# Kernel tuning notes

Hardware: AMD Instinct MI355X
Metric: run time of the kernel (lower is better)

The kernel has to match this reference:

```python
import jax, jax.numpy as jnp
import numpy as np

HEAD = 16
EMB = 1024
D_K = EMB // HEAD


def setup_inputs() -> dict:
    key = jax.random.key(0)
    ks = jax.random.split(key, 11)
    B, S, E = 2, 2048, EMB
    scale = 1.0 / np.sqrt(E)
    inp = {
        "query": jax.random.normal(ks[0], (B, S, E), jnp.float32),
        "key": jax.random.normal(ks[1], (B, S, E), jnp.float32),
        "value": jax.random.normal(ks[2], (B, S, E), jnp.float32),
        "Wq": jax.random.normal(ks[3], (E, E), jnp.float32) * scale,
        "bq": jnp.zeros((E,), jnp.float32),
        "Wk": jax.random.normal(ks[4], (E, E), jnp.float32) * scale,
        "bk": jnp.zeros((E,), jnp.float32),
        "Wv": jax.random.normal(ks[5], (E, E), jnp.float32) * scale,
        "bv": jnp.zeros((E,), jnp.float32),
        "Wo": jax.random.normal(ks[6], (E, E), jnp.float32) * scale,
        "bo": jnp.zeros((E,), jnp.float32),
    }
    return inp


def reference(query, key, value, Wq, bq, Wk, bk, Wv, bv, Wo, bo):
    B, S, E = query.shape
    # 3 input projections, split into heads: [B, H, S, d_k]
    def proj(x, W, b):
        return (x @ W.T + b).reshape(B, S, HEAD, D_K).transpose(0, 2, 1, 3)

    q = proj(query, Wq, bq)
    k = proj(key, Wk, bk)
    v = proj(value, Wv, bv)

    # scaled dot-product attention (full matrix, as in original)
    scores = jnp.einsum("bhqd,bhkd->bhqk", q, k) / jnp.sqrt(jnp.float32(D_K))
    attn = jax.nn.softmax(scores, axis=-1)  # dropout in eval mode = identity
    x = jnp.einsum("bhqk,bhkd->bhqd", attn, v)

    # merge heads and output projection
    x = x.transpose(0, 2, 1, 3).reshape(B, S, E)
    return x @ Wo.T + bo
```

## Files before the change

### kernel.cpp

```cpp
#include <hip/hip_runtime.h>
#include <hip/hip_bf16.h>
#include <math.h>


constexpr int Sn = 2048;
constexpr int En = 1024;
constexpr int Hn = 16;
constexpr int Dk = 64;
constexpr int Kn = 1024;
constexpr size_t WSZ = 1048576;
constexpr size_t TSZ = 4194304;
constexpr int PST = 72;

typedef __bf16 bf16x8 __attribute__((ext_vector_type(8)));
typedef float  f32x4  __attribute__((ext_vector_type(4)));

union U16 { uint4 u; bf16x8 v; __hip_bfloat16 h[8]; };
union U8  { uint2 u; __hip_bfloat162 h2[2]; __hip_bfloat16 h[4]; };

__device__ inline U16 cvt8f(const float* __restrict__ p) {
    float4 a = *(const float4*)p;
    float4 b = *(const float4*)(p + 4);
    U16 r;
    r.h[0] = __float2bfloat16(a.x); r.h[1] = __float2bfloat16(a.y);
    r.h[2] = __float2bfloat16(a.z); r.h[3] = __float2bfloat16(a.w);
    r.h[4] = __float2bfloat16(b.x); r.h[5] = __float2bfloat16(b.y);
    r.h[6] = __float2bfloat16(b.z); r.h[7] = __float2bfloat16(b.w);
    return r;
}

__device__ inline void gload16(const __hip_bfloat16* g, __hip_bfloat16* l) {
    __builtin_amdgcn_global_load_lds(
        (const __attribute__((address_space(1))) void*)g,
        (__attribute__((address_space(3))) void*)l, 16, 0, 0);
}

template<int ROWS, int NW>
__device__ inline void stage_tile(const __hip_bfloat16* __restrict__ src, int ld,
                                  __hip_bfloat16* lds, int w, int lane) {
    int l8 = lane >> 3;
    int g = (lane & 7) ^ (l8 & 7);
    #pragma unroll
    for (int j = 0; j < ROWS / (8 * NW); ++j) {
        int c = j * NW + w;
        gload16(src + (size_t)(c * 8 + l8) * ld + g * 8, lds + c * 512);
    }
}

__global__ __launch_bounds__(256)
void cvt_w(const float* __restrict__ w0, const float* __restrict__ w1,
           const float* __restrict__ w2, const float* __restrict__ w3,
           __hip_bfloat16* __restrict__ dst)
{
    int y = blockIdx.y;
    const float* src = (y == 0) ? w0 : (y == 1) ? w1 : (y == 2) ? w2 : w3;
    size_t i = ((size_t)blockIdx.x * 256 + threadIdx.x) * 8;
    U16 r = cvt8f(src + i);
    *(uint4*)&dst[(size_t)y * WSZ + i] = r.u;
}

__global__ __launch_bounds__(256)
void qkv_gemm(const float* __restrict__ xq, const float* __restrict__ xk,
              const float* __restrict__ xv, const __hip_bfloat16* __restrict__ Wbf,
              const float* __restrict__ bq, const float* __restrict__ bk,
              const float* __restrict__ bv,
              __hip_bfloat16* __restrict__ Qw, __hip_bfloat16* __restrict__ Kw,
              __hip_bfloat16* __restrict__ Vtw)
{
    __shared__ __align__(16) __hip_bfloat16 As[128 * 64];
    __shared__ __align__(16) __hip_bfloat16 Bs[128 * 64];

    const int tid = threadIdx.x, w = tid >> 6, lane = tid & 63;
    const int l15 = lane & 15, lg = lane >> 4, l7 = lane & 7;
    const int z = blockIdx.z;
    const float* A    = (z == 0) ? xq : (z == 1) ? xk : xv;
    const float* bias = (z == 0) ? bq : (z == 1) ? bk : bv;
    const __hip_bfloat16* W = Wbf + (size_t)z * WSZ;
    const int blockM = blockIdx.x * 128, blockN = blockIdx.y * 128;
    const int wm = (w & 1) * 64, wn = (w >> 1) * 64;

    const int arow = tid >> 1, acb = (tid & 1) * 4;
    const int coff0 = (lg ^ l7) * 8;
    const int coff1 = ((4 + lg) ^ l7) * 8;

    f32x4 acc[4][4];
    #pragma unroll
    for (int i = 0; i < 4; ++i)
        #pragma unroll
        for (int j = 0; j < 4; ++j) acc[i][j] = {0.f, 0.f, 0.f, 0.f};

    for (int k0 = 0; k0 < Kn; k0 += 64) {
        {
            const float* ap = A + (size_t)(blockM + arow) * Kn + k0 + acb * 8;
            int s7 = arow & 7;
            #pragma unroll
            for (int g = 0; g < 4; ++g) {
                U16 r = cvt8f(ap + g * 8);
                *(uint4*)&As[arow * 64 + (((acb + g) ^ s7) * 8)] = r.u;
            }
        }
        stage_tile<128, 4>(W + (size_t)blockN * Kn + k0, Kn, Bs, w, lane);
        __syncthreads();

        U16 af[4][2], bf[4][2];
        #pragma unroll
        for (int mt = 0; mt < 4; ++mt) {
            int r = (wm + mt * 16 + l15) * 64;
            af[mt][0].u = *(const uint4*)&As[r + coff0];
            af[mt][1].u = *(const uint4*)&As[r + coff1];
        }
        #pragma unroll
        for (int nt = 0; nt < 4; ++nt) {
            int r = (wn + nt * 16 + l15) * 64;
            bf[nt][0].u = *(const uint4*)&Bs[r + coff0];
            bf[nt][1].u = *(const uint4*)&Bs[r + coff1];
        }
        #pragma unroll
        for (int mt = 0; mt < 4; ++mt)
            #pragma unroll
            for (int nt = 0; nt < 4; ++nt) {
                acc[mt][nt] = __builtin_amdgcn_mfma_f32_16x16x32_bf16(af[mt][0].v, bf[nt][0].v, acc[mt][nt], 0, 0, 0);
                acc[mt][nt] = __builtin_amdgcn_mfma_f32_16x16x32_bf16(af[mt][1].v, bf[nt][1].v, acc[mt][nt], 0, 0, 0);
            }
        __syncthreads();
    }

    #pragma unroll
    for (int nt = 0; nt < 4; ++nt) {
        int n = blockN + wn + nt * 16 + l15;
        float bvn = bias[n];
        int h_ = n >> 6, d_ = n & 63;
        #pragma unroll
        for (int mt = 0; mt < 4; ++mt) {
            int m0 = blockM + wm + mt * 16 + lg * 4;
            int b_ = m0 >> 11, s_ = m0 & (Sn - 1);
            if (z == 2) {
                U8 pk;
                #pragma unroll
                for (int i = 0; i < 4; ++i) pk.h[i] = __float2bfloat16(acc[mt][nt][i] + bvn);
                *(uint2*)&Vtw[(((size_t)b_ * Hn + h_) * Dk + d_) * Sn + s_] = pk.u;
            } else {
                __hip_bfloat16* D = (z == 0) ? Qw : Kw;
                #pragma unroll
                for (int i = 0; i < 4; ++i)
                    D[(((size_t)b_ * Hn + h_) * Sn + s_ + i) * Dk + d_] =
                        __float2bfloat16(acc[mt][nt][i] + bvn);
            }
        }
    }
}

__global__ __launch_bounds__(256)
void fin_gemm(const __hip_bfloat16* __restrict__ A, const __hip_bfloat16* __restrict__ W,
              const float* __restrict__ bias, float* __restrict__ out)
{
    __shared__ __align__(16) __hip_bfloat16 As[128 * 64];
    __shared__ __align__(16) __hip_bfloat16 Bs[128 * 64];

    const int tid = threadIdx.x, w = tid >> 6, lane = tid & 63;
    const int l15 = lane & 15, lg = lane >> 4, l7 = lane & 7;
    const int blockM = blockIdx.x * 128, blockN = blockIdx.y * 128;
    const int wm = (w & 1) * 64, wn = (w >> 1) * 64;
    const int coff0 = (lg ^ l7) * 8;
    const int coff1 = ((4 + lg) ^ l7) * 8;

    f32x4 acc[4][4];
    #pragma unroll
    for (int i = 0; i < 4; ++i)
        #pragma unroll
        for (int j = 0; j < 4; ++j) acc[i][j] = {0.f, 0.f, 0.f, 0.f};

    for (int k0 = 0; k0 < Kn; k0 += 64) {
        stage_tile<128, 4>(A + (size_t)blockM * Kn + k0, Kn, As, w, lane);
        stage_tile<128, 4>(W + (size_t)blockN * Kn + k0, Kn, Bs, w, lane);
        __syncthreads();

        U16 af[4][2], bf[4][2];
        #pragma unroll
        for (int mt = 0; mt < 4; ++mt) {
            int r = (wm + mt * 16 + l15) * 64;
            af[mt][0].u = *(const uint4*)&As[r + coff0];
            af[mt][1].u = *(const uint4*)&As[r + coff1];
        }
        #pragma unroll
        for (int nt = 0; nt < 4; ++nt) {
            int r = (wn + nt * 16 + l15) * 64;
            bf[nt][0].u = *(const uint4*)&Bs[r + coff0];
            bf[nt][1].u = *(const uint4*)&Bs[r + coff1];
        }
        #pragma unroll
        for (int mt = 0; mt < 4; ++mt)
            #pragma unroll
            for (int nt = 0; nt < 4; ++nt) {
                acc[mt][nt] = __builtin_amdgcn_mfma_f32_16x16x32_bf16(af[mt][0].v, bf[nt][0].v, acc[mt][nt], 0, 0, 0);
                acc[mt][nt] = __builtin_amdgcn_mfma_f32_16x16x32_bf16(af[mt][1].v, bf[nt][1].v, acc[mt][nt], 0, 0, 0);
            }
        __syncthreads();
    }

    #pragma unroll
    for (int nt = 0; nt < 4; ++nt) {
        int n = blockN + wn + nt * 16 + l15;
        float bvn = bias[n];
        #pragma unroll
        for (int mt = 0; mt < 4; ++mt) {
            int m0 = blockM + wm + mt * 16 + lg * 4;
            #pragma unroll
            for (int i = 0; i < 4; ++i)
                out[(size_t)(m0 + i) * Kn + n] = acc[mt][nt][i] + bvn;
        }
    }
}

__global__ __launch_bounds__(256)
void attn(const __hip_bfloat16* __restrict__ Q, const __hip_bfloat16* __restrict__ K,
          const __hip_bfloat16* __restrict__ Vt, __hip_bfloat16* __restrict__ X)
{
    __shared__ __align__(16) __hip_bfloat16 Ks[64 * 64];
    __shared__ __align__(16) __hip_bfloat16 Vts[64 * 64];
    __shared__ __align__(16) __hip_bfloat16 Ps[128 * PST];

    const int bh = blockIdx.y, q0 = blockIdx.x * 128;
    const int tid = threadIdx.x, w = tid >> 6, lane = tid & 63;
    const int l15 = lane & 15, lg = lane >> 4, l7 = lane & 7;
    const int coff0 = (lg ^ l7) * 8;
    const int coff1 = ((4 + lg) ^ l7) * 8;

    const __hip_bfloat16* Qb = Q  + (size_t)bh * Sn * Dk;
    const __hip_bfloat16* Kb = K  + (size_t)bh * Sn * Dk;
    const __hip_bfloat16* Vb = Vt + (size_t)bh * Dk * Sn;

    U16 aq[2][2];
    #pragma unroll
    for (int qt = 0; qt < 2; ++qt) {
        const __hip_bfloat16* qp = Qb + (size_t)(q0 + w * 32 + qt * 16 + l15) * Dk + lg * 8;
        aq[qt][0].u = *(const uint4*)qp;
        aq[qt][1].u = *(const uint4*)(qp + 32);
    }

    f32x4 o[2][4];
    float lpart[2];
    #pragma unroll
    for (int qt = 0; qt < 2; ++qt) {
        lpart[qt] = 0.f;
        #pragma unroll
        for (int dt = 0; dt < 4; ++dt) o[qt][dt] = {0.f, 0.f, 0.f, 0.f};
    }

    __hip_bfloat16* Pw = Ps + (w * 32) * PST;

    for (int k0 = 0; k0 < Sn; k0 += 64) {
        stage_tile<64, 4>(Kb + (size_t)k0 * Dk, Dk, Ks, w, lane);
        stage_tile<64, 4>(Vb + k0, Sn, Vts, w, lane);
        __syncthreads();

        U16 kf[4][2];
        #pragma unroll
        for (int kt = 0; kt < 4; ++kt) {
            int r = (kt * 16 + l15) * 64;
            kf[kt][0].u = *(const uint4*)&Ks[r + coff0];
            kf[kt][1].u = *(const uint4*)&Ks[r + coff1];
        }
        #pragma unroll
        for (int kt = 0; kt < 4; ++kt)
            #pragma unroll
            for (int qt = 0; qt < 2; ++qt) {
                f32x4 s = {0.f, 0.f, 0.f, 0.f};
                s = __builtin_amdgcn_mfma_f32_16x16x32_bf16(kf[kt][0].v, aq[qt][0].v, s, 0, 0, 0);
                s = __builtin_amdgcn_mfma_f32_16x16x32_bf16(kf[kt][1].v, aq[qt][1].v, s, 0, 0, 0);
                float p0 = __expf(s[0] * 0.125f), p1 = __expf(s[1] * 0.125f);
                float p2 = __expf(s[2] * 0.125f), p3 = __expf(s[3] * 0.125f);
                lpart[qt] += (p0 + p1) + (p2 + p3);
                U8 pk;
                pk.h2[0] = __float22bfloat162_rn({p0, p1});
                pk.h2[1] = __float22bfloat162_rn({p2, p3});
                *(uint2*)&Pw[(qt * 16 + l15) * PST + kt * 16 + lg * 4] = pk.u;
            }

        U16 pf[2][2], vf[4][2];
        #pragma unroll
        for (int qt = 0; qt < 2; ++qt) {
            const __hip_bfloat16* pr = &Pw[(qt * 16 + l15) * PST + lg * 8];
            pf[qt][0].u = *(const uint4*)pr;
            pf[qt][1].u = *(const uint4*)(pr + 32);
        }
        #pragma unroll
        for (int dt = 0; dt < 4; ++dt) {
            int r = (dt * 16 + l15) * 64;
            vf[dt][0].u = *(const uint4*)&Vts[r + coff0];
            vf[dt][1].u = *(const uint4*)&Vts[r + coff1];
        }
        #pragma unroll
        for (int qt = 0; qt < 2; ++qt)
            #pragma unroll
            for (int dt = 0; dt < 4; ++dt) {
                o[qt][dt] = __builtin_amdgcn_mfma_f32_16x16x32_bf16(pf[qt][0].v, vf[dt][0].v, o[qt][dt], 0, 0, 0);
                o[qt][dt] = __builtin_amdgcn_mfma_f32_16x16x32_bf16(pf[qt][1].v, vf[dt][1].v, o[qt][dt], 0, 0, 0);
            }
        __syncthreads();
    }

    float linv[2][4];
    #pragma unroll
    for (int qt = 0; qt < 2; ++qt) {
        float v = lpart[qt];
        v += __shfl_xor(v, 16, 64);
        v += __shfl_xor(v, 32, 64);
        #pragma unroll
        for (int i = 0; i < 4; ++i)
            linv[qt][i] = 1.f / __shfl(v, lg * 4 + i, 16);
    }

    int b_ = bh >> 4, h_ = bh & (Hn - 1);
    #pragma unroll
    for (int qt = 0; qt < 2; ++qt)
        #pragma unroll
        for (int i = 0; i < 4; ++i) {
            int sr = q0 + w * 32 + qt * 16 + lg * 4 + i;
            __hip_bfloat16* xp = X + ((size_t)(b_ * Sn + sr)) * En + h_ * Dk + l15;
            #pragma unroll
            for (int dt = 0; dt < 4; ++dt)
                xp[dt * 16] = __float2bfloat16(o[qt][dt][i] * linv[qt][i]);
        }
}

extern "C" void kernel_launch(void* const* d_in, const int* in_sizes, int n_in,
                              void* d_out, int out_size, void* d_ws, size_t ws_size,
                              hipStream_t stream)
{
    const float* query = (const float*)d_in[0];
    const float* key   = (const float*)d_in[1];
    const float* value = (const float*)d_in[2];
    const float* Wq = (const float*)d_in[3];
    const float* bq = (const float*)d_in[4];
    const float* Wk = (const float*)d_in[5];
    const float* bk = (const float*)d_in[6];
    const float* Wv = (const float*)d_in[7];
    const float* bv = (const float*)d_in[8];
    const float* Wo = (const float*)d_in[9];
    const float* bo = (const float*)d_in[10];
    float* out = (float*)d_out;

    __hip_bfloat16* Wbf = (__hip_bfloat16*)d_ws;
    __hip_bfloat16* Qw  = Wbf + 4 * WSZ;
    __hip_bfloat16* Kw  = Qw + TSZ;
    __hip_bfloat16* Vtw = Kw + TSZ;
    __hip_bfloat16* Xw  = Vtw + TSZ;

    cvt_w<<<dim3(512, 4), 256, 0, stream>>>(Wq, Wk, Wv, Wo, Wbf);
    qkv_gemm<<<dim3(32, 8, 3), 256, 0, stream>>>(query, key, value, Wbf,
                                                 bq, bk, bv, Qw, Kw, Vtw);
    attn<<<dim3(Sn / 128, 32), 256, 0, stream>>>(Qw, Kw, Vtw, Xw);
    fin_gemm<<<dim3(32, 8), 256, 0, stream>>>(Xw, Wbf + 3 * WSZ, bo, out);
}
```

Measured before the change: 272.5 us.

## Pre-convert activations to bf16, shrink GEMM tiles, double-buffer attention K/V

Activations are converted to bf16 by a separate kernel, one input at a time, before the projections. The projections and output GEMM now share a templated 64x128-tile GEMM that stages both operands directly, which doubles the block count for better CU fill. The attention kernel double-buffers its K/V shared-memory tiles so the next tile loads while the current one computes, dropping one barrier per iteration. The cost is extra kernel launches, serialized projection GEMMs that each launch only 512 blocks, and extra global traffic for the bf16 activation copies.

```diff
diff --git a/kernel.cpp b/kernel.cpp
--- a/kernel.cpp
+++ b/kernel.cpp
@@ -60,51 +60,42 @@
 }
 
 __global__ __launch_bounds__(256)
-void qkv_gemm(const float* __restrict__ xq, const float* __restrict__ xk,
-              const float* __restrict__ xv, const __hip_bfloat16* __restrict__ Wbf,
-              const float* __restrict__ bq, const float* __restrict__ bk,
-              const float* __restrict__ bv,
-              __hip_bfloat16* __restrict__ Qw, __hip_bfloat16* __restrict__ Kw,
-              __hip_bfloat16* __restrict__ Vtw)
-{
-    __shared__ __align__(16) __hip_bfloat16 As[128 * 64];
+void cvt_x(const float* __restrict__ src, __hip_bfloat16* __restrict__ dst)
+{
+    size_t i = ((size_t)blockIdx.x * 256 + threadIdx.x) * 8;
+    U16 r = cvt8f(src + i);
+    *(uint4*)&dst[i] = r.u;
+}
+
+template<int MODE>
+__global__ __launch_bounds__(256)
+void gemm64(const __hip_bfloat16* __restrict__ A, const __hip_bfloat16* __restrict__ W,
+            const float* __restrict__ bias, void* __restrict__ outp)
+{
+    __shared__ __align__(16) __hip_bfloat16 As[64 * 64];
     __shared__ __align__(16) __hip_bfloat16 Bs[128 * 64];
 
     const int tid = threadIdx.x, w = tid >> 6, lane = tid & 63;
     const int l15 = lane & 15, lg = lane >> 4, l7 = lane & 7;
-    const int z = blockIdx.z;
-    const float* A    = (z == 0) ? xq : (z == 1) ? xk : xv;
-    const float* bias = (z == 0) ? bq : (z == 1) ? bk : bv;
-    const __hip_bfloat16* W = Wbf + (size_t)z * WSZ;
-    const int blockM = blockIdx.x * 128, blockN = blockIdx.y * 128;
-    const int wm = (w & 1) * 64, wn = (w >> 1) * 64;
-
-    const int arow = tid >> 1, acb = (tid & 1) * 4;
+    const int blockM = blockIdx.x * 64, blockN = blockIdx.y * 128;
+    const int wm = (w & 1) * 32, wn = (w >> 1) * 64;
     const int coff0 = (lg ^ l7) * 8;
     const int coff1 = ((4 + lg) ^ l7) * 8;
 
-    f32x4 acc[4][4];
-    #pragma unroll
-    for (int i = 0; i < 4; ++i)
+    f32x4 acc[2][4];
+    #pragma unroll
+    for (int i = 0; i < 2; ++i)
         #pragma unroll
         for (int j = 0; j < 4; ++j) acc[i][j] = {0.f, 0.f, 0.f, 0.f};
 
     for (int k0 = 0; k0 < Kn; k0 += 64) {
-        {
-            const float* ap = A + (size_t)(blockM + arow) * Kn + k0 + acb * 8;
-            int s7 = arow & 7;
-            #pragma unroll
-            for (int g = 0; g < 4; ++g) {
-                U16 r = cvt8f(ap + g * 8);
-                *(uint4*)&As[arow * 64 + (((acb + g) ^ s7) * 8)] = r.u;
-            }
-        }
+        stage_tile<64, 4>(A + (size_t)blockM * Kn + k0, Kn, As, w, lane);
         stage_tile<128, 4>(W + (size_t)blockN * Kn + k0, Kn, Bs, w, lane);
         __syncthreads();
 
-        U16 af[4][2], bf[4][2];
-        #pragma unroll
-        for (int mt = 0; mt < 4; ++mt) {
+        U16 af[2][2], bf[4][2];
+        #pragma unroll
+        for (int mt = 0; mt < 2; ++mt) {
             int r = (wm + mt * 16 + l15) * 64;
             af[mt][0].u = *(const uint4*)&As[r + coff0];
             af[mt][1].u = *(const uint4*)&As[r + coff1];
@@ -116,7 +107,7 @@
             bf[nt][1].u = *(const uint4*)&Bs[r + coff1];
         }
         #pragma unroll
-        for (int mt = 0; mt < 4; ++mt)
+        for (int mt = 0; mt < 2; ++mt)
             #pragma unroll
             for (int nt = 0; nt < 4; ++nt) {
                 acc[mt][nt] = __builtin_amdgcn_mfma_f32_16x16x32_bf16(af[mt][0].v, bf[nt][0].v, acc[mt][nt], 0, 0, 0);
@@ -131,83 +122,28 @@
         float bvn = bias[n];
         int h_ = n >> 6, d_ = n & 63;
         #pragma unroll
-        for (int mt = 0; mt < 4; ++mt) {
+        for (int mt = 0; mt < 2; ++mt) {
             int m0 = blockM + wm + mt * 16 + lg * 4;
-            int b_ = m0 >> 11, s_ = m0 & (Sn - 1);
-            if (z == 2) {
+            if constexpr (MODE == 0) {
+                float* out = (float*)outp;
+                #pragma unroll
+                for (int i = 0; i < 4; ++i)
+                    out[(size_t)(m0 + i) * Kn + n] = acc[mt][nt][i] + bvn;
+            } else if constexpr (MODE == 1) {
+                __hip_bfloat16* out = (__hip_bfloat16*)outp;
+                int b_ = m0 >> 11, s_ = m0 & (Sn - 1);
+                #pragma unroll
+                for (int i = 0; i < 4; ++i)
+                    out[(((size_t)b_ * Hn + h_) * Sn + s_ + i) * Dk + d_] =
+                        __float2bfloat16(acc[mt][nt][i] + bvn);
+            } else {
+                __hip_bfloat16* out = (__hip_bfloat16*)outp;
+                int b_ = m0 >> 11, s_ = m0 & (Sn - 1);
                 U8 pk;
                 #pragma unroll
                 for (int i = 0; i < 4; ++i) pk.h[i] = __float2bfloat16(acc[mt][nt][i] + bvn);
-                *(uint2*)&Vtw[(((size_t)b_ * Hn + h_) * Dk + d_) * Sn + s_] = pk.u;
-            } else {
-                __hip_bfloat16* D = (z == 0) ? Qw : Kw;
-                #pragma unroll
-                for (int i = 0; i < 4; ++i)
-                    D[(((size_t)b_ * Hn + h_) * Sn + s_ + i) * Dk + d_] =
-                        __float2bfloat16(acc[mt][nt][i] + bvn);
+                *(uint2*)&out[(((size_t)b_ * Hn + h_) * Dk + d_) * Sn + s_] = pk.u;
             }
-        }
-    }
-}
-
-__global__ __launch_bounds__(256)
-void fin_gemm(const __hip_bfloat16* __restrict__ A, const __hip_bfloat16* __restrict__ W,
-              const float* __restrict__ bias, float* __restrict__ out)
-{
-    __shared__ __align__(16) __hip_bfloat16 As[128 * 64];
-    __shared__ __align__(16) __hip_bfloat16 Bs[128 * 64];
-
-    const int tid = threadIdx.x, w = tid >> 6, lane = tid & 63;
-    const int l15 = lane & 15, lg = lane >> 4, l7 = lane & 7;
-    const int blockM = blockIdx.x * 128, blockN = blockIdx.y * 128;
-    const int wm = (w & 1) * 64, wn = (w >> 1) * 64;
-    const int coff0 = (lg ^ l7) * 8;
-    const int coff1 = ((4 + lg) ^ l7) * 8;
-
-    f32x4 acc[4][4];
-    #pragma unroll
-    for (int i = 0; i < 4; ++i)
-        #pragma unroll
-        for (int j = 0; j < 4; ++j) acc[i][j] = {0.f, 0.f, 0.f, 0.f};
-
-    for (int k0 = 0; k0 < Kn; k0 += 64) {
-        stage_tile<128, 4>(A + (size_t)blockM * Kn + k0, Kn, As, w, lane);
-        stage_tile<128, 4>(W + (size_t)blockN * Kn + k0, Kn, Bs, w, lane);
-        __syncthreads();
-
-        U16 af[4][2], bf[4][2];
-        #pragma unroll
-        for (int mt = 0; mt < 4; ++mt) {
-            int r = (wm + mt * 16 + l15) * 64;
-            af[mt][0].u = *(const uint4*)&As[r + coff0];
-            af[mt][1].u = *(const uint4*)&As[r + coff1];
-        }
-        #pragma unroll
-        for (int nt = 0; nt < 4; ++nt) {
-            int r = (wn + nt * 16 + l15) * 64;
-            bf[nt][0].u = *(const uint4*)&Bs[r + coff0];
-            bf[nt][1].u = *(const uint4*)&Bs[r + coff1];
-        }
-        #pragma unroll
-        for (int mt = 0; mt < 4; ++mt)
-            #pragma unroll
-            for (int nt = 0; nt < 4; ++nt) {
-                acc[mt][nt] = __builtin_amdgcn_mfma_f32_16x16x32_bf16(af[mt][0].v, bf[nt][0].v, acc[mt][nt], 0, 0, 0);
-                acc[mt][nt] = __builtin_amdgcn_mfma_f32_16x16x32_bf16(af[mt][1].v, bf[nt][1].v, acc[mt][nt], 0, 0, 0);
-            }
-        __syncthreads();
-    }
-
-    #pragma unroll
-    for (int nt = 0; nt < 4; ++nt) {
-        int n = blockN + wn + nt * 16 + l15;
-        float bvn = bias[n];
-        #pragma unroll
-        for (int mt = 0; mt < 4; ++mt) {
-            int m0 = blockM + wm + mt * 16 + lg * 4;
-            #pragma unroll
-            for (int i = 0; i < 4; ++i)
-                out[(size_t)(m0 + i) * Kn + n] = acc[mt][nt][i] + bvn;
         }
     }
 }
@@ -216,8 +152,8 @@
 void attn(const __hip_bfloat16* __restrict__ Q, const __hip_bfloat16* __restrict__ K,
           const __hip_bfloat16* __restrict__ Vt, __hip_bfloat16* __restrict__ X)
 {
-    __shared__ __align__(16) __hip_bfloat16 Ks[64 * 64];
-    __shared__ __align__(16) __hip_bfloat16 Vts[64 * 64];
+    __shared__ __align__(16) __hip_bfloat16 Ks[2][64 * 64];
+    __shared__ __align__(16) __hip_bfloat16 Vts[2][64 * 64];
     __shared__ __align__(16) __hip_bfloat16 Ps[128 * PST];
 
     const int bh = blockIdx.y, q0 = blockIdx.x * 128;
@@ -249,17 +185,23 @@
 
     __hip_bfloat16* Pw = Ps + (w * 32) * PST;
 
-    for (int k0 = 0; k0 < Sn; k0 += 64) {
-        stage_tile<64, 4>(Kb + (size_t)k0 * Dk, Dk, Ks, w, lane);
-        stage_tile<64, 4>(Vb + k0, Sn, Vts, w, lane);
+    stage_tile<64, 4>(Kb, Dk, Ks[0], w, lane);
+    stage_tile<64, 4>(Vb, Sn, Vts[0], w, lane);
+
+    for (int t = 0; t < Sn / 64; ++t) {
         __syncthreads();
+        const int cur = t & 1;
+        if (t + 1 < Sn / 64) {
+            stage_tile<64, 4>(Kb + (size_t)(t + 1) * 64 * Dk, Dk, Ks[cur ^ 1], w, lane);
+            stage_tile<64, 4>(Vb + (t + 1) * 64, Sn, Vts[cur ^ 1], w, lane);
+        }
 
         U16 kf[4][2];
         #pragma unroll
         for (int kt = 0; kt < 4; ++kt) {
             int r = (kt * 16 + l15) * 64;
-            kf[kt][0].u = *(const uint4*)&Ks[r + coff0];
-            kf[kt][1].u = *(const uint4*)&Ks[r + coff1];
+            kf[kt][0].u = *(const uint4*)&Ks[cur][r + coff0];
+            kf[kt][1].u = *(const uint4*)&Ks[cur][r + coff1];
         }
         #pragma unroll
         for (int kt = 0; kt < 4; ++kt)
@@ -287,8 +229,8 @@
         #pragma unroll
         for (int dt = 0; dt < 4; ++dt) {
             int r = (dt * 16 + l15) * 64;
-            vf[dt][0].u = *(const uint4*)&Vts[r + coff0];
-            vf[dt][1].u = *(const uint4*)&Vts[r + coff1];
+            vf[dt][0].u = *(const uint4*)&Vts[cur][r + coff0];
+            vf[dt][1].u = *(const uint4*)&Vts[cur][r + coff1];
         }
         #pragma unroll
         for (int qt = 0; qt < 2; ++qt)
@@ -297,7 +239,6 @@
                 o[qt][dt] = __builtin_amdgcn_mfma_f32_16x16x32_bf16(pf[qt][0].v, vf[dt][0].v, o[qt][dt], 0, 0, 0);
                 o[qt][dt] = __builtin_amdgcn_mfma_f32_16x16x32_bf16(pf[qt][1].v, vf[dt][1].v, o[qt][dt], 0, 0, 0);
             }
-        __syncthreads();
     }
 
     float linv[2][4];
@@ -341,15 +282,22 @@
     const float* bo = (const float*)d_in[10];
     float* out = (float*)d_out;
 
-    __hip_bfloat16* Wbf = (__hip_bfloat16*)d_ws;
-    __hip_bfloat16* Qw  = Wbf + 4 * WSZ;
-    __hip_bfloat16* Kw  = Qw + TSZ;
-    __hip_bfloat16* Vtw = Kw + TSZ;
-    __hip_bfloat16* Xw  = Vtw + TSZ;
+    __hip_bfloat16* xbuf = (__hip_bfloat16*)d_ws;
+    __hip_bfloat16* Wbf  = xbuf + TSZ;
+    __hip_bfloat16* Qw   = Wbf + 4 * WSZ;
+    __hip_bfloat16* Kw   = Qw + TSZ;
+    __hip_bfloat16* Vtw  = Kw + TSZ;
+    __hip_bfloat16* Xw   = xbuf;
+
+    dim3 ggrid(64, 8);
 
     cvt_w<<<dim3(512, 4), 256, 0, stream>>>(Wq, Wk, Wv, Wo, Wbf);
-    qkv_gemm<<<dim3(32, 8, 3), 256, 0, stream>>>(query, key, value, Wbf,
-                                                 bq, bk, bv, Qw, Kw, Vtw);
+    cvt_x<<<2048, 256, 0, stream>>>(query, xbuf);
+    gemm64<1><<<ggrid, 256, 0, stream>>>(xbuf, Wbf, bq, Qw);
+    cvt_x<<<2048, 256, 0, stream>>>(key, xbuf);
+    gemm64<1><<<ggrid, 256, 0, stream>>>(xbuf, Wbf + WSZ, bk, Kw);
+    cvt_x<<<2048, 256, 0, stream>>>(value, xbuf);
+    gemm64<2><<<ggrid, 256, 0, stream>>>(xbuf, Wbf + 2 * WSZ, bv, Vtw);
     attn<<<dim3(Sn / 128, 32), 256, 0, stream>>>(Qw, Kw, Vtw, Xw);
-    fin_gemm<<<dim3(32, 8), 256, 0, stream>>>(Xw, Wbf + 3 * WSZ, bo, out);
-}
+    gemm64<0><<<ggrid, 256, 0, stream>>>(Xw, Wbf + 3 * WSZ, bo, out);
+}
```

Measured after the change: 245.5 us. 9.9% less time.
